# Optimization experiments

Hardware: AMD Instinct MI355X
Metric: run time of the kernel (lower is better)

The kernel has to match this reference:

```python
import jax, jax.numpy as jnp
import numpy as np

HEADS = 16
KEY_SIZE = 64
SIZE_PER_HEAD = 64
OUT_DIM = HEADS * SIZE_PER_HEAD  # 1024
BIG = 1e10
B, LQ, LK = 2, 2048, 2048


def setup_inputs() -> dict:
    key = jax.random.key(0)
    ks = jax.random.split(key, 8)
    q = jax.random.normal(ks[0], (B, LQ, OUT_DIM), dtype=jnp.float32)
    k = jax.random.normal(ks[1], (B, LK, OUT_DIM), dtype=jnp.float32)
    v = jax.random.normal(ks[2], (B, LK, OUT_DIM), dtype=jnp.float32)
    v_mask = (jax.random.uniform(ks[3], (B, LK)) > 0.1).astype(jnp.float32)
    q_mask = (jax.random.uniform(ks[4], (B, LQ)) > 0.1).astype(jnp.float32)
    # bias-free Linear weights, torch layout [out_features, in_features]
    s = 1.0 / np.sqrt(OUT_DIM)
    Wq = jax.random.normal(ks[5], (HEADS * KEY_SIZE, OUT_DIM), dtype=jnp.float32) * s
    Wk = jax.random.normal(ks[6], (HEADS * KEY_SIZE, OUT_DIM), dtype=jnp.float32) * s
    Wv = jax.random.normal(ks[7], (OUT_DIM, OUT_DIM), dtype=jnp.float32) * s
    return {"q": q, "k": k, "v": v, "v_mask": v_mask, "q_mask": q_mask,
            "Wq": Wq, "Wk": Wk, "Wv": Wv}


def _attention(q, k, v, v_mask, q_mask, Wq, Wk, Wv):
    b, lq, _ = q.shape
    lk = k.shape[1]
    # projections (torch Linear: x @ W.T)
    qw = jnp.einsum('bld,ed->ble', q, Wq).reshape(b, lq, HEADS, KEY_SIZE)
    kw = jnp.einsum('bld,ed->ble', k, Wk).reshape(b, lk, HEADS, KEY_SIZE)
    vw = jnp.einsum('bld,ed->ble', v, Wv).reshape(b, lk, HEADS, SIZE_PER_HEAD)
    # scores [B, H, Lq, Lk]
    a = jnp.einsum('bqhd,bkhd->bhqk', qw, kw) / np.sqrt(KEY_SIZE).astype(np.float32)
    # additive key-padding mask: a - (1 - v_mask) * BIG, broadcast over H and Lq
    a = a - (1.0 - v_mask)[:, None, None, :] * BIG
    # mask_right=True branch: mask = (1 - triu(ones, diag=1)) * BIG, i.e. lower
    # triangle INCLUDING the diagonal is penalized (faithful to source quirk).
    causal = jnp.tril(jnp.ones((lq, lk), dtype=a.dtype)) * BIG  # [Lq, Lk]
    a = a - causal[None, None, :, :]
    a = jax.nn.softmax(a, axis=-1)
    # output [B, Lq, H*dv]
    o = jnp.einsum('bhqk,bkhd->bqhd', a, vw).reshape(b, lq, OUT_DIM)
    o = o * q_mask[:, :, None]
    return o


def reference(q, k, v, v_mask, q_mask, Wq, Wk, Wv):
    return _attention(q, k, v, v_mask, q_mask, Wq, Wk, Wv)
```

## Files before the change

kernel.cpp:

```cpp
#include <hip/hip_runtime.h>
#include <hip/hip_bf16.h>
#include <stdint.h>

#define B_    2
#define SEQ   2048
#define EMB   1024
#define BIGF  1e10f
#define LOG2E 1.4426950408889634f
#define BIG2F (1e10f * LOG2E)
#define C2    (0.125f * LOG2E)

typedef unsigned short u16;
typedef __attribute__((ext_vector_type(4))) u16      u16x4;
typedef __attribute__((ext_vector_type(8))) short    bf8;
typedef __attribute__((ext_vector_type(4))) float    f4;
typedef __attribute__((ext_vector_type(4))) float    fv4;

__device__ inline float bf2f(u16 u){ union{uint32_t i; float f;} v; v.i = ((uint32_t)u) << 16; return v.f; }
__device__ inline u16 f2bf(float f){ union{float f; uint32_t i;} v; v.f = f;
                                     uint32_t r = v.i + 0x7fffu + ((v.i >> 16) & 1u); return (u16)(r >> 16); }
__device__ inline float exp2_hw(float x){ float r; asm("v_exp_f32 %0, %1" : "=v"(r) : "v"(x)); return r; }

__device__ inline void gl_lds16(const void* g, void* l){
  __builtin_amdgcn_global_load_lds((const __attribute__((address_space(1))) uint32_t*)g,
                                   (__attribute__((address_space(3))) uint32_t*)l, 16, 0, 0);
}

struct CvtArgs { const float* src[6]; u16* dst[6]; int n[6]; };

__global__ __launch_bounds__(256) void cvt_bf16(CvtArgs a)
{
  const int seg = blockIdx.y;
  const float* __restrict__ s = a.src[seg];
  u16* __restrict__ d = a.dst[seg];
  const int n = a.n[seg];
  const int i = (blockIdx.x * 256 + threadIdx.x) * 8;
  if (i >= n) return;
  fv4 x0 = *(const fv4*)(s + i);
  fv4 x1 = *(const fv4*)(s + i + 4);
  union { bf8 v; u16 u[8]; } o;
#pragma unroll
  for (int j = 0; j < 4; j++) { o.u[j] = f2bf(x0[j]); o.u[4 + j] = f2bf(x1[j]); }
  *(bf8*)(d + i) = o.v;
}

__global__ __launch_bounds__(256) void proj_gemm(
    const u16* __restrict__ Xq, const u16* __restrict__ Xk, const u16* __restrict__ Xv,
    const u16* __restrict__ Wq, const u16* __restrict__ Wk, const u16* __restrict__ Wv,
    u16* __restrict__ QH, u16* __restrict__ KH, u16* __restrict__ VTB)
{
  __shared__ u16 smem[24576];
  const int z = blockIdx.z;
  const u16* X = (z == 0) ? Xq : ((z == 1) ? Xk : Xv);
  const u16* W = (z == 0) ? Wq : ((z == 1) ? Wk : Wv);

  const int tid  = threadIdx.x;
  const int lane = tid & 63;
  const int w    = tid >> 6;
  const int wm   = w >> 1, wn = w & 1;
  const int m0   = blockIdx.x * 128;
  const int n0   = blockIdx.y * 128;
  const int col  = lane & 15, quad = lane >> 4;
  const int sq8  = (quad ^ ((col >> 1) & 3)) * 8;

  const int srow = w * 16 + (lane >> 2);
  const int sc   = ((lane & 3) ^ ((lane >> 3) & 3)) * 8;
  const size_t gA0 = (size_t)(m0 + srow) * 1024 + sc;
  const size_t gA1 = (size_t)(m0 + 64 + srow) * 1024 + sc;
  const size_t gB0 = (size_t)(n0 + srow) * 1024 + sc;
  const size_t gB1 = (size_t)(n0 + 64 + srow) * 1024 + sc;
  const int ldst = w * 512 + lane * 8;

#define PSTAGE(nb, kn) do { \
    gl_lds16(X + gA0 + (kn), &(nb)[ldst]); \
    gl_lds16(X + gA1 + (kn), &(nb)[2048 + ldst]); \
    gl_lds16(W + gB0 + (kn), &(nb)[4096 + ldst]); \
    gl_lds16(W + gB1 + (kn), &(nb)[6144 + ldst]); \
  } while (0)

  const f4 zero = {0.f, 0.f, 0.f, 0.f};
  f4 acc[4][4];
#pragma unroll
  for (int i = 0; i < 4; i++)
#pragma unroll
    for (int j = 0; j < 4; j++) acc[i][j] = zero;

  PSTAGE(smem, 0);
  PSTAGE((smem + 8192), 32);
  PSTAGE((smem + 16384), 64);

#define PBODY(T, BASE, DOSTAGE) do { \
    __builtin_amdgcn_s_barrier(); \
    __builtin_amdgcn_sched_barrier(0); \
    const u16* cA_ = (BASE); \
    const u16* cB_ = (BASE) + 4096; \
    bf8 a_[4], b_[4]; \
    _Pragma("unroll") \
    for (int tt = 0; tt < 4; tt++) a_[tt] = *(const bf8*)&cA_[(wm * 64 + tt * 16 + col) * 32 + sq8]; \
    _Pragma("unroll") \
    for (int tt = 0; tt < 4; tt++) b_[tt] = *(const bf8*)&cB_[(wn * 64 + tt * 16 + col) * 32 + sq8]; \
    asm volatile("s_waitcnt lgkmcnt(0)" ::: "memory"); \
    __builtin_amdgcn_sched_barrier(0); \
    __builtin_amdgcn_s_barrier(); \
    if (DOSTAGE) { PSTAGE((BASE), ((T) + 3) * 32); } \
    __builtin_amdgcn_s_setprio(1); \
    _Pragma("unroll") \
    for (int mt = 0; mt < 4; mt++) \
      _Pragma("unroll") \
      for (int nt = 0; nt < 4; nt++) \
        acc[mt][nt] = __builtin_amdgcn_mfma_f32_16x16x32_bf16(a_[mt], b_[nt], acc[mt][nt], 0, 0, 0); \
    __builtin_amdgcn_s_setprio(0); \
  } while (0)

  for (int t3 = 0; t3 < 27; t3 += 3) {
    asm volatile("s_waitcnt vmcnt(8)" ::: "memory"); PBODY(t3 + 0, smem, 1);
    asm volatile("s_waitcnt vmcnt(8)" ::: "memory"); PBODY(t3 + 1, (smem + 8192), 1);
    asm volatile("s_waitcnt vmcnt(8)" ::: "memory"); PBODY(t3 + 2, (smem + 16384), 1);
  }
  asm volatile("s_waitcnt vmcnt(8)" ::: "memory"); PBODY(27, smem, 1);
  asm volatile("s_waitcnt vmcnt(8)" ::: "memory"); PBODY(28, (smem + 8192), 1);
  asm volatile("s_waitcnt vmcnt(8)" ::: "memory"); PBODY(29, (smem + 16384), 0);
  asm volatile("s_waitcnt vmcnt(4)" ::: "memory"); PBODY(30, smem, 0);
  asm volatile("s_waitcnt vmcnt(0)" ::: "memory"); PBODY(31, (smem + 8192), 0);
#undef PBODY
#undef PSTAGE

  __syncthreads();
  u16* ep = &smem[w * 4608];

  if (z == 2) {
#pragma unroll
    for (int mt = 0; mt < 4; mt++)
#pragma unroll
      for (int nt = 0; nt < 4; nt++) {
        u16x4 pk = { f2bf(acc[mt][nt][0]), f2bf(acc[mt][nt][1]),
                     f2bf(acc[mt][nt][2]), f2bf(acc[mt][nt][3]) };
        *(u16x4*)&ep[(nt * 16 + col) * 72 + mt * 16 + quad * 4] = pk;
      }
  } else {
#pragma unroll
    for (int mt = 0; mt < 4; mt++)
#pragma unroll
      for (int nt = 0; nt < 4; nt++)
#pragma unroll
        for (int r = 0; r < 4; r++)
          ep[(mt * 16 + quad * 4 + r) * 72 + nt * 16 + col] = f2bf(acc[mt][nt][r]);
  }

  const int bb = m0 >> 11;
  const int h  = (n0 >> 6) + wn;
  const int bh = bb * 16 + h;

  if (z == 0) {
    const int qbase = (m0 & 2047) + wm * 64;
    u16* dst = QH + ((size_t)bh * SEQ + qbase) * 64;
#pragma unroll
    for (int i = 0; i < 8; i++) {
      const int f  = i * 1024 + lane * 16;
      const int ml = i * 8 + (lane >> 3), nl = (lane & 7) * 8;
      *(bf8*)(dst + (f >> 1)) = *(const bf8*)&ep[ml * 72 + nl];
    }
  } else if (z == 1) {
    const int kt = (((m0 & 2047) >> 6) + wm);
    u16* dst = KH + (((size_t)bh * 32 + kt) << 12);
#pragma unroll
    for (int i = 0; i < 8; i++) {
      const int f   = i * 1024 + lane * 16;
      const int dh  = f >> 12;
      const int klc = (f >> 6) & 63;
      const int dlo = (lane & 3) * 8;
      const int fs  = f ^ (((klc >> 1) & 3) << 4);
      *(bf8*)(dst + (fs >> 1)) = *(const bf8*)&ep[klc * 72 + dh * 32 + dlo];
    }
  } else {
    const int kt = (((m0 & 2047) >> 6) + wm);
    u16* dst = VTB + (((size_t)bh * 32 + kt) << 12);
#pragma unroll
    for (int i = 0; i < 8; i++) {
      const int f   = i * 1024 + lane * 16;
      const int kk  = f >> 12;
      const int d   = (f >> 6) & 63;
      const int klo = (lane & 3) * 8;
      const int fs  = f ^ (((d >> 1) & 3) << 4);
      *(bf8*)(dst + (fs >> 1)) = *(const bf8*)&ep[d * 72 + kk * 32 + klo];
    }
  }
}

__global__ __launch_bounds__(256) void sumv(const u16* __restrict__ VTB,
                                            const float* __restrict__ vmask,
                                            float* __restrict__ fb)
{
  const int w = threadIdx.x >> 6, lane = threadIdx.x & 63;
  const int gw = blockIdx.x * 4 + w;
  const int b = gw >> 10, e = gw & 1023;
  const int h = e >> 6, d = e & 63;
  const int bh = b * 16 + h;
  const float* vm = vmask + b * SEQ;
  const int ksw = (lane & 31) ^ (((d >> 1) & 3) << 3);
  float s = 0.f, c = 0.f;
  for (int kt = 0; kt < 32; kt++) {
    const u16 val = VTB[(((size_t)bh * 32 + kt) << 12) + (lane >> 5) * 2048 + d * 32 + ksw];
    const float m = vm[kt * 64 + lane];
    s += m * bf2f(val); c += m;
  }
#pragma unroll
  for (int o = 1; o < 64; o <<= 1) { s += __shfl_xor(s, o); c += __shfl_xor(c, o); }
  if (lane == 0) fb[gw] = s / c;
}

__global__ __launch_bounds__(256) void attn(
    const u16* __restrict__ QH, const u16* __restrict__ KH, const u16* __restrict__ VTB,
    const float* __restrict__ vmask, const float* __restrict__ qmask,
    const float* __restrict__ fb, float* __restrict__ OUT)
{
  __shared__ float pen[SEQ];
  __shared__ u16   sK[2][4096];
  __shared__ u16   sV[2][4096];
  __shared__ u16   P[4 * 16 * 72];

  const int tid = threadIdx.x, lane = tid & 63, w = tid >> 6;
  const int i   = blockIdx.x;
  const int xcd = i & 7;
  const int j   = i >> 3;
  const int qx  = j >> 2;
  const int bh  = xcd + 8 * (j & 3);
  const int b = bh >> 4, h = bh & 15;
  const int col = lane & 15, quad = lane >> 4;
  const int sq8 = (quad ^ ((col >> 1) & 3)) * 8;
  const int wb = w * 16 * 72;

  for (int t = tid; t < SEQ; t += 256)
    pen[t] = (1.0f - vmask[b * SEQ + t]) * BIG2F;

  const u16* kbase = KH  + (((size_t)bh * 32) << 12);
  const u16* vbase = VTB + (((size_t)bh * 32) << 12);

  const int q0 = qx * 64;

  bf8 bQ[2];
#pragma unroll
  for (int dh = 0; dh < 2; dh++)
    bQ[dh] = *(const bf8*)&QH[((size_t)bh * SEQ + q0 + w * 16 + col) * 64 + dh * 32 + quad * 8];

  const f4 zero = {0.f, 0.f, 0.f, 0.f};
  f4 accO[4];
  float l_acc = 0.f;
#pragma unroll
  for (int t = 0; t < 4; t++) accO[t] = zero;

#define ASTAGE(BUF, KT) do { \
    const size_t toff_ = ((size_t)(KT) << 12) + w * 1024 + lane * 8; \
    gl_lds16(kbase + toff_,       &sK[(BUF)][w * 1024]); \
    gl_lds16(kbase + toff_ + 512, &sK[(BUF)][w * 1024 + 512]); \
    gl_lds16(vbase + toff_,       &sV[(BUF)][w * 1024]); \
    gl_lds16(vbase + toff_ + 512, &sV[(BUF)][w * 1024 + 512]); \
  } while (0)

  const int ntile = 32 - qx;
  ASTAGE(0, qx);
  ASTAGE(1, qx + 1);

  for (int it = 0; it < ntile; it++) {
    if (it + 1 < ntile) asm volatile("s_waitcnt vmcnt(4) lgkmcnt(0)" ::: "memory");
    else                asm volatile("s_waitcnt vmcnt(0) lgkmcnt(0)" ::: "memory");
    __builtin_amdgcn_s_barrier();
    __builtin_amdgcn_sched_barrier(0);

    const u16* cK = sK[it & 1];
    const u16* cV = sV[it & 1];
    const int k0 = (qx + it) * 64;

    fv4 pv[4];
#pragma unroll
    for (int nt = 0; nt < 4; nt++) pv[nt] = *(const fv4*)&pen[k0 + nt * 16 + quad * 4];

    f4 accS[4];
#pragma unroll
    for (int t = 0; t < 4; t++) accS[t] = zero;
    __builtin_amdgcn_s_setprio(1);
#pragma unroll
    for (int nt = 0; nt < 4; nt++)
#pragma unroll
      for (int dh = 0; dh < 2; dh++) {
        bf8 aK = *(const bf8*)&cK[dh * 2048 + (nt * 16 + col) * 32 + sq8];
        accS[nt] = __builtin_amdgcn_mfma_f32_16x16x32_bf16(aK, bQ[dh], accS[nt], 0, 0, 0);
      }
    __builtin_amdgcn_s_setprio(0);

    float p[4][4];
    if (it == 0) {
#pragma unroll
      for (int nt = 0; nt < 4; nt++)
#pragma unroll
        for (int r = 0; r < 4; r++) {
          float sv = fmaf(accS[nt][r], C2, -pv[nt][r]);
          if (nt * 16 + quad * 4 + r <= w * 16 + col) sv -= BIG2F;
          p[nt][r] = exp2_hw(sv);
        }
    } else {
#pragma unroll
      for (int nt = 0; nt < 4; nt++)
#pragma unroll
        for (int r = 0; r < 4; r++)
          p[nt][r] = exp2_hw(fmaf(accS[nt][r], C2, -pv[nt][r]));
    }
#pragma unroll
    for (int nt = 0; nt < 4; nt++)
      l_acc += (p[nt][0] + p[nt][1]) + (p[nt][2] + p[nt][3]);

#pragma unroll
    for (int nt = 0; nt < 4; nt++) {
      union { u16x4 v; u16 u[4]; } pk;
      union { __hip_bfloat162 h2; u16 u[2]; } c0, c1;
      float2 f01; f01.x = p[nt][0]; f01.y = p[nt][1];
      float2 f23; f23.x = p[nt][2]; f23.y = p[nt][3];
      c0.h2 = __float22bfloat162_rn(f01);
      c1.h2 = __float22bfloat162_rn(f23);
      pk.u[0] = c0.u[0]; pk.u[1] = c0.u[1]; pk.u[2] = c1.u[0]; pk.u[3] = c1.u[1];
      *(u16x4*)&P[wb + col * 72 + nt * 16 + quad * 4] = pk.v;
    }

    __builtin_amdgcn_s_setprio(1);
#pragma unroll
    for (int kk = 0; kk < 2; kk++) {
      bf8 bP = *(const bf8*)&P[wb + col * 72 + kk * 32 + quad * 8];
#pragma unroll
      for (int nt = 0; nt < 4; nt++) {
        bf8 aV = *(const bf8*)&cV[kk * 2048 + (nt * 16 + col) * 32 + sq8];
        accO[nt] = __builtin_amdgcn_mfma_f32_16x16x32_bf16(aV, bP, accO[nt], 0, 0, 0);
      }
    }
    __builtin_amdgcn_s_setprio(0);

    asm volatile("s_waitcnt lgkmcnt(0)" ::: "memory");
    __builtin_amdgcn_sched_barrier(0);
    __builtin_amdgcn_s_barrier();
    if (it + 2 < ntile) { ASTAGE((it & 1), qx + it + 2); }
  }
#undef ASTAGE

  float l = l_acc;
  l += __shfl_xor(l, 16); l += __shfl_xor(l, 32);
  const int q = q0 + w * 16 + col;
  const float qm = qmask[b * SEQ + q];
  float* op = OUT + (size_t)(b * SEQ + q) * EMB + h * 64;
  if (l == 0.0f) {
#pragma unroll
    for (int nt = 0; nt < 4; nt++) {
      fv4 f = *(const fv4*)&fb[b * 1024 + h * 64 + nt * 16 + quad * 4];
      f *= qm;
      *(fv4*)(op + nt * 16 + quad * 4) = f;
    }
  } else {
    const float s = qm / l;
#pragma unroll
    for (int nt = 0; nt < 4; nt++) {
      fv4 f = { accO[nt][0] * s, accO[nt][1] * s, accO[nt][2] * s, accO[nt][3] * s };
      *(fv4*)(op + nt * 16 + quad * 4) = f;
    }
  }
}

extern "C" void kernel_launch(void* const* d_in, const int* in_sizes, int n_in,
                              void* d_out, int out_size, void* d_ws, size_t ws_size,
                              hipStream_t stream)
{
  const float* q  = (const float*)d_in[0];
  const float* k  = (const float*)d_in[1];
  const float* v  = (const float*)d_in[2];
  const float* vm = (const float*)d_in[3];
  const float* qm = (const float*)d_in[4];
  const float* Wq = (const float*)d_in[5];
  const float* Wk = (const float*)d_in[6];
  const float* Wv = (const float*)d_in[7];
  float* out = (float*)d_out;

  const size_t NBIG = (size_t)B_ * SEQ * EMB;
  const size_t NW   = (size_t)EMB * EMB;

  u16* qb  = (u16*)d_ws;
  u16* kb  = qb  + NBIG;
  u16* vb  = kb  + NBIG;
  u16* Wqb = vb  + NBIG;
  u16* Wkb = Wqb + NW;
  u16* Wvb = Wkb + NW;
  u16* QH  = Wvb + NW;
  u16* KH  = QH  + NBIG;
  u16* VTB = KH  + NBIG;
  float* fb = (float*)(VTB + NBIG);

  CvtArgs ca;
  ca.src[0] = q;  ca.dst[0] = qb;  ca.n[0] = (int)NBIG;
  ca.src[1] = k;  ca.dst[1] = kb;  ca.n[1] = (int)NBIG;
  ca.src[2] = v;  ca.dst[2] = vb;  ca.n[2] = (int)NBIG;
  ca.src[3] = Wq; ca.dst[3] = Wqb; ca.n[3] = (int)NW;
  ca.src[4] = Wk; ca.dst[4] = Wkb; ca.n[4] = (int)NW;
  ca.src[5] = Wv; ca.dst[5] = Wvb; ca.n[5] = (int)NW;

  cvt_bf16<<<dim3((unsigned)(NBIG / 8 / 256), 6, 1), 256, 0, stream>>>(ca);
  proj_gemm<<<dim3(32, 8, 3), 256, 0, stream>>>(qb, kb, vb, Wqb, Wkb, Wvb, QH, KH, VTB);
  sumv<<<dim3(512, 1, 1), 256, 0, stream>>>(VTB, vm, fb);
  attn<<<dim3(1024, 1, 1), 256, 0, stream>>>(QH, KH, VTB, vm, qm, fb, out);
}
```

Before: 178.8 us.

## Precompute key-padding penalty globally, prefetch into registers, shrink LDS for occupancy

Moves the per-block key-mask penalty computation into the sumv kernel as a global array. The attention kernel then prefetches the next tile's penalty values from global memory into registers, one iteration ahead, rather than holding an 8KB LDS copy. The P scratch buffer drops its padding and uses an XOR-swizzled layout to avoid bank conflicts, and launch bounds now request 4 blocks per CU. Less LDS per block should let more blocks stay resident, at the cost of extra global loads and register pressure under the tighter register budget.

```diff
diff --git a/kernel.cpp b/kernel.cpp
--- a/kernel.cpp
+++ b/kernel.cpp
@@ -189,8 +189,14 @@
 
 __global__ __launch_bounds__(256) void sumv(const u16* __restrict__ VTB,
                                             const float* __restrict__ vmask,
-                                            float* __restrict__ fb)
+                                            float* __restrict__ fb,
+                                            float* __restrict__ peng)
 {
+  if (blockIdx.x < 16) {
+    const int g = blockIdx.x * 256 + threadIdx.x;
+    peng[g] = (1.0f - vmask[g]) * BIG2F;
+  }
+
   const int w = threadIdx.x >> 6, lane = threadIdx.x & 63;
   const int gw = blockIdx.x * 4 + w;
   const int b = gw >> 10, e = gw & 1023;
@@ -209,15 +215,14 @@
   if (lane == 0) fb[gw] = s / c;
 }
 
-__global__ __launch_bounds__(256) void attn(
+__global__ __launch_bounds__(256, 4) void attn(
     const u16* __restrict__ QH, const u16* __restrict__ KH, const u16* __restrict__ VTB,
-    const float* __restrict__ vmask, const float* __restrict__ qmask,
+    const float* __restrict__ peng, const float* __restrict__ qmask,
     const float* __restrict__ fb, float* __restrict__ OUT)
 {
-  __shared__ float pen[SEQ];
-  __shared__ u16   sK[2][4096];
-  __shared__ u16   sV[2][4096];
-  __shared__ u16   P[4 * 16 * 72];
+  __shared__ u16 sK[2][4096];
+  __shared__ u16 sV[2][4096];
+  __shared__ u16 P[4 * 16 * 64];
 
   const int tid = threadIdx.x, lane = tid & 63, w = tid >> 6;
   const int i   = blockIdx.x;
@@ -228,13 +233,12 @@
   const int b = bh >> 4, h = bh & 15;
   const int col = lane & 15, quad = lane >> 4;
   const int sq8 = (quad ^ ((col >> 1) & 3)) * 8;
-  const int wb = w * 16 * 72;
-
-  for (int t = tid; t < SEQ; t += 256)
-    pen[t] = (1.0f - vmask[b * SEQ + t]) * BIG2F;
+  const int wb  = w * 1024;
+  const int c7  = col & 7;
 
   const u16* kbase = KH  + (((size_t)bh * 32) << 12);
   const u16* vbase = VTB + (((size_t)bh * 32) << 12);
+  const float* pg  = peng + b * SEQ;
 
   const int q0 = qx * 64;
 
@@ -258,6 +262,10 @@
   } while (0)
 
   const int ntile = 32 - qx;
+  fv4 pvc0 = *(const fv4*)&pg[q0 + quad * 4];
+  fv4 pvc1 = *(const fv4*)&pg[q0 + 16 + quad * 4];
+  fv4 pvc2 = *(const fv4*)&pg[q0 + 32 + quad * 4];
+  fv4 pvc3 = *(const fv4*)&pg[q0 + 48 + quad * 4];
   ASTAGE(0, qx);
   ASTAGE(1, qx + 1);
 
@@ -269,11 +277,15 @@
 
     const u16* cK = sK[it & 1];
     const u16* cV = sV[it & 1];
-    const int k0 = (qx + it) * 64;
-
-    fv4 pv[4];
-#pragma unroll
-    for (int nt = 0; nt < 4; nt++) pv[nt] = *(const fv4*)&pen[k0 + nt * 16 + quad * 4];
+
+    fv4 pvn0, pvn1, pvn2, pvn3;
+    if (it + 1 < ntile) {
+      const int kn = (qx + it + 1) * 64;
+      pvn0 = *(const fv4*)&pg[kn + quad * 4];
+      pvn1 = *(const fv4*)&pg[kn + 16 + quad * 4];
+      pvn2 = *(const fv4*)&pg[kn + 32 + quad * 4];
+      pvn3 = *(const fv4*)&pg[kn + 48 + quad * 4];
+    }
 
     f4 accS[4];
 #pragma unroll
@@ -291,19 +303,23 @@
     float p[4][4];
     if (it == 0) {
 #pragma unroll
-      for (int nt = 0; nt < 4; nt++)
+      for (int nt = 0; nt < 4; nt++) {
+        const fv4 pv = (nt == 0) ? pvc0 : ((nt == 1) ? pvc1 : ((nt == 2) ? pvc2 : pvc3));
 #pragma unroll
         for (int r = 0; r < 4; r++) {
-          float sv = fmaf(accS[nt][r], C2, -pv[nt][r]);
+          float sv = fmaf(accS[nt][r], C2, -pv[r]);
           if (nt * 16 + quad * 4 + r <= w * 16 + col) sv -= BIG2F;
           p[nt][r] = exp2_hw(sv);
         }
+      }
     } else {
 #pragma unroll
-      for (int nt = 0; nt < 4; nt++)
+      for (int nt = 0; nt < 4; nt++) {
+        const fv4 pv = (nt == 0) ? pvc0 : ((nt == 1) ? pvc1 : ((nt == 2) ? pvc2 : pvc3));
 #pragma unroll
         for (int r = 0; r < 4; r++)
-          p[nt][r] = exp2_hw(fmaf(accS[nt][r], C2, -pv[nt][r]));
+          p[nt][r] = exp2_hw(fmaf(accS[nt][r], C2, -pv[r]));
+      }
     }
 #pragma unroll
     for (int nt = 0; nt < 4; nt++)
@@ -312,19 +328,21 @@
 #pragma unroll
     for (int nt = 0; nt < 4; nt++) {
       union { u16x4 v; u16 u[4]; } pk;
-      union { __hip_bfloat162 h2; u16 u[2]; } c0, c1;
+      union { __hip_bfloat162 h2; u16 u[2]; } cc0, cc1;
       float2 f01; f01.x = p[nt][0]; f01.y = p[nt][1];
       float2 f23; f23.x = p[nt][2]; f23.y = p[nt][3];
-      c0.h2 = __float22bfloat162_rn(f01);
-      c1.h2 = __float22bfloat162_rn(f23);
-      pk.u[0] = c0.u[0]; pk.u[1] = c0.u[1]; pk.u[2] = c1.u[0]; pk.u[3] = c1.u[1];
-      *(u16x4*)&P[wb + col * 72 + nt * 16 + quad * 4] = pk.v;
+      cc0.h2 = __float22bfloat162_rn(f01);
+      cc1.h2 = __float22bfloat162_rn(f23);
+      pk.u[0] = cc0.u[0]; pk.u[1] = cc0.u[1]; pk.u[2] = cc1.u[0]; pk.u[3] = cc1.u[1];
+      const int ch = (2 * nt + (quad >> 1)) ^ c7;
+      *(u16x4*)&P[wb + col * 64 + ch * 8 + (quad & 1) * 4] = pk.v;
     }
 
     __builtin_amdgcn_s_setprio(1);
 #pragma unroll
     for (int kk = 0; kk < 2; kk++) {
-      bf8 bP = *(const bf8*)&P[wb + col * 72 + kk * 32 + quad * 8];
+      const int rch = (kk * 4 + quad) ^ c7;
+      bf8 bP = *(const bf8*)&P[wb + col * 64 + rch * 8];
 #pragma unroll
       for (int nt = 0; nt < 4; nt++) {
         bf8 aV = *(const bf8*)&cV[kk * 2048 + (nt * 16 + col) * 32 + sq8];
@@ -332,6 +350,8 @@
       }
     }
     __builtin_amdgcn_s_setprio(0);
+
+    pvc0 = pvn0; pvc1 = pvn1; pvc2 = pvn2; pvc3 = pvn3;
 
     asm volatile("s_waitcnt lgkmcnt(0)" ::: "memory");
     __builtin_amdgcn_sched_barrier(0);
@@ -388,7 +408,8 @@
   u16* QH  = Wvb + NW;
   u16* KH  = QH  + NBIG;
   u16* VTB = KH  + NBIG;
-  float* fb = (float*)(VTB + NBIG);
+  float* fb   = (float*)(VTB + NBIG);
+  float* peng = fb + 2048;
 
   CvtArgs ca;
   ca.src[0] = q;  ca.dst[0] = qb;  ca.n[0] = (int)NBIG;
@@ -400,6 +421,6 @@
 
   cvt_bf16<<<dim3((unsigned)(NBIG / 8 / 256), 6, 1), 256, 0, stream>>>(ca);
   proj_gemm<<<dim3(32, 8, 3), 256, 0, stream>>>(qb, kb, vb, Wqb, Wkb, Wvb, QH, KH, VTB);
-  sumv<<<dim3(512, 1, 1), 256, 0, stream>>>(VTB, vm, fb);
-  attn<<<dim3(1024, 1, 1), 256, 0, stream>>>(QH, KH, VTB, vm, qm, fb, out);
-}
+  sumv<<<dim3(512, 1, 1), 256, 0, stream>>>(VTB, vm, fb, peng);
+  attn<<<dim3(1024, 1, 1), 256, 0, stream>>>(QH, KH, VTB, peng, qm, fb, out);
+}
```

New measurement: 182.0 us. Within noise of the previous version (+1.8%).

## Fuse fp32-to-bf16 activation conversion into projection GEMM loads

Applied to the files above, without the earlier changes.

The separate conversion pass over the q/k/v activations is removed. The projection GEMM now streams fp32 activations directly into LDS and converts them to bf16 in registers before the MFMAs, while only the weights still go through the conversion kernel. This avoids writing and re-reading about 25 MB of bf16 intermediates. In exchange the A tile doubles in LDS size, the pipeline drops from three stages to two, and occupancy is hinted with launch bounds (256,3). Scalar bf16 rounding is also replaced with the packed __float22bfloat162_rn intrinsic.

```diff
diff --git a/kernel.cpp b/kernel.cpp
--- a/kernel.cpp
+++ b/kernel.cpp
@@ -26,7 +26,18 @@
                                    (__attribute__((address_space(3))) uint32_t*)l, 16, 0, 0);
 }
 
-struct CvtArgs { const float* src[6]; u16* dst[6]; int n[6]; };
+__device__ inline bf8 pack8(fv4 a, fv4 b){
+  union { bf8 v; u16 u[8]; } o;
+  union { __hip_bfloat162 h2; u16 u[2]; } c;
+  float2 t;
+  t.x = a[0]; t.y = a[1]; c.h2 = __float22bfloat162_rn(t); o.u[0] = c.u[0]; o.u[1] = c.u[1];
+  t.x = a[2]; t.y = a[3]; c.h2 = __float22bfloat162_rn(t); o.u[2] = c.u[0]; o.u[3] = c.u[1];
+  t.x = b[0]; t.y = b[1]; c.h2 = __float22bfloat162_rn(t); o.u[4] = c.u[0]; o.u[5] = c.u[1];
+  t.x = b[2]; t.y = b[3]; c.h2 = __float22bfloat162_rn(t); o.u[6] = c.u[0]; o.u[7] = c.u[1];
+  return o.v;
+}
+
+struct CvtArgs { const float* src[3]; u16* dst[3]; int n[3]; };
 
 __global__ __launch_bounds__(256) void cvt_bf16(CvtArgs a)
 {
@@ -38,21 +49,18 @@
   if (i >= n) return;
   fv4 x0 = *(const fv4*)(s + i);
   fv4 x1 = *(const fv4*)(s + i + 4);
-  union { bf8 v; u16 u[8]; } o;
-#pragma unroll
-  for (int j = 0; j < 4; j++) { o.u[j] = f2bf(x0[j]); o.u[4 + j] = f2bf(x1[j]); }
-  *(bf8*)(d + i) = o.v;
-}
-
-__global__ __launch_bounds__(256) void proj_gemm(
-    const u16* __restrict__ Xq, const u16* __restrict__ Xk, const u16* __restrict__ Xv,
+  *(bf8*)(d + i) = pack8(x0, x1);
+}
+
+__global__ __launch_bounds__(256, 3) void proj_gemm(
+    const float* __restrict__ Xq, const float* __restrict__ Xk, const float* __restrict__ Xv,
     const u16* __restrict__ Wq, const u16* __restrict__ Wk, const u16* __restrict__ Wv,
     u16* __restrict__ QH, u16* __restrict__ KH, u16* __restrict__ VTB)
 {
   __shared__ u16 smem[24576];
   const int z = blockIdx.z;
-  const u16* X = (z == 0) ? Xq : ((z == 1) ? Xk : Xv);
-  const u16* W = (z == 0) ? Wq : ((z == 1) ? Wk : Wv);
+  const float* X = (z == 0) ? Xq : ((z == 1) ? Xk : Xv);
+  const u16*   W = (z == 0) ? Wq : ((z == 1) ? Wk : Wv);
 
   const int tid  = threadIdx.x;
   const int lane = tid & 63;
@@ -63,19 +71,25 @@
   const int col  = lane & 15, quad = lane >> 4;
   const int sq8  = (quad ^ ((col >> 1) & 3)) * 8;
 
+  const int rA  = tid >> 3;
+  const int cAe = ((tid & 7) ^ (rA & 7)) * 4;
+  const size_t gAb = (size_t)(m0 + rA) * 1024 + cAe;
+
+  const int aIdx = ((wm * 64 + col) * 128 + (((quad * 2) ^ (col & 7)) * 16)) >> 1;
+
   const int srow = w * 16 + (lane >> 2);
   const int sc   = ((lane & 3) ^ ((lane >> 3) & 3)) * 8;
-  const size_t gA0 = (size_t)(m0 + srow) * 1024 + sc;
-  const size_t gA1 = (size_t)(m0 + 64 + srow) * 1024 + sc;
   const size_t gB0 = (size_t)(n0 + srow) * 1024 + sc;
   const size_t gB1 = (size_t)(n0 + 64 + srow) * 1024 + sc;
   const int ldst = w * 512 + lane * 8;
 
 #define PSTAGE(nb, kn) do { \
-    gl_lds16(X + gA0 + (kn), &(nb)[ldst]); \
-    gl_lds16(X + gA1 + (kn), &(nb)[2048 + ldst]); \
-    gl_lds16(W + gB0 + (kn), &(nb)[4096 + ldst]); \
-    gl_lds16(W + gB1 + (kn), &(nb)[6144 + ldst]); \
+    gl_lds16(X + gAb + (kn),         &(nb)[tid * 8]); \
+    gl_lds16(X + gAb + 32768 + (kn), &(nb)[2048 + tid * 8]); \
+    gl_lds16(X + gAb + 65536 + (kn), &(nb)[4096 + tid * 8]); \
+    gl_lds16(X + gAb + 98304 + (kn), &(nb)[6144 + tid * 8]); \
+    gl_lds16(W + gB0 + (kn),         &(nb)[8192 + ldst]); \
+    gl_lds16(W + gB1 + (kn),         &(nb)[10240 + ldst]); \
   } while (0)
 
   const f4 zero = {0.f, 0.f, 0.f, 0.f};
@@ -86,23 +100,30 @@
     for (int j = 0; j < 4; j++) acc[i][j] = zero;
 
   PSTAGE(smem, 0);
-  PSTAGE((smem + 8192), 32);
-  PSTAGE((smem + 16384), 64);
-
-#define PBODY(T, BASE, DOSTAGE) do { \
+  PSTAGE((smem + 12288), 32);
+
+#define PBODY(T, BASE, DOSTAGE, WAITN) do { \
+    asm volatile("s_waitcnt vmcnt(" #WAITN ")" ::: "memory"); \
     __builtin_amdgcn_s_barrier(); \
     __builtin_amdgcn_sched_barrier(0); \
     const u16* cA_ = (BASE); \
-    const u16* cB_ = (BASE) + 4096; \
-    bf8 a_[4], b_[4]; \
+    const u16* cB_ = (BASE) + 8192; \
+    fv4 xa0[4], xa1[4]; \
+    bf8 b_[4]; \
     _Pragma("unroll") \
-    for (int tt = 0; tt < 4; tt++) a_[tt] = *(const bf8*)&cA_[(wm * 64 + tt * 16 + col) * 32 + sq8]; \
+    for (int tt = 0; tt < 4; tt++) { \
+      xa0[tt] = *(const fv4*)&cA_[aIdx + tt * 1024]; \
+      xa1[tt] = *(const fv4*)&cA_[(aIdx + tt * 1024) ^ 8]; \
+    } \
     _Pragma("unroll") \
     for (int tt = 0; tt < 4; tt++) b_[tt] = *(const bf8*)&cB_[(wn * 64 + tt * 16 + col) * 32 + sq8]; \
     asm volatile("s_waitcnt lgkmcnt(0)" ::: "memory"); \
     __builtin_amdgcn_sched_barrier(0); \
     __builtin_amdgcn_s_barrier(); \
-    if (DOSTAGE) { PSTAGE((BASE), ((T) + 3) * 32); } \
+    if (DOSTAGE) { PSTAGE((BASE), ((T) + 2) * 32); } \
+    bf8 a_[4]; \
+    _Pragma("unroll") \
+    for (int tt = 0; tt < 4; tt++) a_[tt] = pack8(xa0[tt], xa1[tt]); \
     __builtin_amdgcn_s_setprio(1); \
     _Pragma("unroll") \
     for (int mt = 0; mt < 4; mt++) \
@@ -112,16 +133,12 @@
     __builtin_amdgcn_s_setprio(0); \
   } while (0)
 
-  for (int t3 = 0; t3 < 27; t3 += 3) {
-    asm volatile("s_waitcnt vmcnt(8)" ::: "memory"); PBODY(t3 + 0, smem, 1);
-    asm volatile("s_waitcnt vmcnt(8)" ::: "memory"); PBODY(t3 + 1, (smem + 8192), 1);
-    asm volatile("s_waitcnt vmcnt(8)" ::: "memory"); PBODY(t3 + 2, (smem + 16384), 1);
-  }
-  asm volatile("s_waitcnt vmcnt(8)" ::: "memory"); PBODY(27, smem, 1);
-  asm volatile("s_waitcnt vmcnt(8)" ::: "memory"); PBODY(28, (smem + 8192), 1);
-  asm volatile("s_waitcnt vmcnt(8)" ::: "memory"); PBODY(29, (smem + 16384), 0);
-  asm volatile("s_waitcnt vmcnt(4)" ::: "memory"); PBODY(30, smem, 0);
-  asm volatile("s_waitcnt vmcnt(0)" ::: "memory"); PBODY(31, (smem + 8192), 0);
+  for (int t = 0; t < 30; t++) {
+    u16* base = smem + (t & 1) * 12288;
+    PBODY(t, base, 1, 6);
+  }
+  PBODY(30, smem, 0, 6);
+  PBODY(31, (smem + 12288), 0, 0);
 #undef PBODY
 #undef PSTAGE
 
@@ -379,10 +396,7 @@
   const size_t NBIG = (size_t)B_ * SEQ * EMB;
   const size_t NW   = (size_t)EMB * EMB;
 
-  u16* qb  = (u16*)d_ws;
-  u16* kb  = qb  + NBIG;
-  u16* vb  = kb  + NBIG;
-  u16* Wqb = vb  + NBIG;
+  u16* Wqb = (u16*)d_ws;
   u16* Wkb = Wqb + NW;
   u16* Wvb = Wkb + NW;
   u16* QH  = Wvb + NW;
@@ -391,15 +405,12 @@
   float* fb = (float*)(VTB + NBIG);
 
   CvtArgs ca;
-  ca.src[0] = q;  ca.dst[0] = qb;  ca.n[0] = (int)NBIG;
-  ca.src[1] = k;  ca.dst[1] = kb;  ca.n[1] = (int)NBIG;
-  ca.src[2] = v;  ca.dst[2] = vb;  ca.n[2] = (int)NBIG;
-  ca.src[3] = Wq; ca.dst[3] = Wqb; ca.n[3] = (int)NW;
-  ca.src[4] = Wk; ca.dst[4] = Wkb; ca.n[4] = (int)NW;
-  ca.src[5] = Wv; ca.dst[5] = Wvb; ca.n[5] = (int)NW;
-
-  cvt_bf16<<<dim3((unsigned)(NBIG / 8 / 256), 6, 1), 256, 0, stream>>>(ca);
-  proj_gemm<<<dim3(32, 8, 3), 256, 0, stream>>>(qb, kb, vb, Wqb, Wkb, Wvb, QH, KH, VTB);
+  ca.src[0] = Wq; ca.dst[0] = Wqb; ca.n[0] = (int)NW;
+  ca.src[1] = Wk; ca.dst[1] = Wkb; ca.n[1] = (int)NW;
+  ca.src[2] = Wv; ca.dst[2] = Wvb; ca.n[2] = (int)NW;
+
+  cvt_bf16<<<dim3((unsigned)(NW / 8 / 256), 3, 1), 256, 0, stream>>>(ca);
+  proj_gemm<<<dim3(32, 8, 3), 256, 0, stream>>>(q, k, v, Wqb, Wkb, Wvb, QH, KH, VTB);
   sumv<<<dim3(512, 1, 1), 256, 0, stream>>>(VTB, vm, fb);
   attn<<<dim3(1024, 1, 1), 256, 0, stream>>>(QH, KH, VTB, vm, qm, fb, out);
 }
```

Result: slower. 187.2 us (+4.7%).
